# Performance work log

Measured on AMD Instinct MI355X. Metric: run time of the kernel, lower is better.

Reference implementation:

```python
import jax, jax.numpy as jnp
import numpy as np

MAX_HOPS = 2
N_NODES = 100000
N_EDGES = 1600000
D_FEAT = 64

def setup_inputs() -> dict:
    key = jax.random.key(0)
    k1, k2 = jax.random.split(key)
    x = jax.random.normal(k1, (N_NODES, D_FEAT), dtype=jnp.float32)
    edge_index = jax.random.randint(k2, (2, N_EDGES), 0, N_NODES, dtype=jnp.int64)
    hop_weights = jnp.ones((MAX_HOPS + 1,), dtype=jnp.float32)
    return {"x": x, "edge_index": edge_index, "hop_weights": hop_weights}

def reference(x, edge_index, hop_weights):
    num_nodes = x.shape[0]
    loops = jnp.arange(num_nodes, dtype=edge_index.dtype)
    row = jnp.concatenate([edge_index[0], loops])  # destination of scatter-add
    col = jnp.concatenate([edge_index[1], loops])  # gather source
    # symmetric GCN normalization D^{-1/2} A D^{-1/2} (degree computed over col, as in source)
    deg = jax.ops.segment_sum(jnp.ones_like(col, dtype=x.dtype), col, num_segments=num_nodes)
    deg_inv_sqrt = jnp.where(deg > 0, jax.lax.rsqrt(deg), 0.0)
    norm = deg_inv_sqrt[row] * deg_inv_sqrt[col]  # [E+N]
    w = jax.nn.softmax(hop_weights)
    result = w[0] * x
    current = x
    for hop in range(1, MAX_HOPS + 1):
        messages = current[col] * norm[:, None]  # irregular gather + scale
        current = jax.ops.segment_sum(messages, row, num_segments=num_nodes)  # scatter-add
        result = result + w[hop] * current
    return result
```

## Files before the change

### kernel.cpp

```cpp
#include <hip/hip_runtime.h>

#define NN 100000
#define NE 1600000
#define D 64

#define BKT 256
#define BROWS ((NN + BKT - 1) / BKT)
#define CAP 8192
#define PADCAP 12288
#define P1_NB 1024
#define P1_T 512
#define EPB ((NE + P1_NB - 1) / P1_NB)

typedef unsigned short u16;
typedef unsigned int u32;
typedef unsigned char u8;
typedef __attribute__((ext_vector_type(8))) unsigned short us8;


__device__ __forceinline__ float bf2f(u16 u) {
    union { u32 i; float f; } x; x.i = ((u32)u) << 16; return x.f;
}
__device__ __forceinline__ u16 f2bf(float f) {
    union { float f; u32 i; } x; x.f = f;
    u32 r = x.i + 0x7FFF + ((x.i >> 16) & 1);
    return (u16)(r >> 16);
}

__global__ void setup_kernel(const float* __restrict__ hw, float* __restrict__ wsm,
                             int* __restrict__ bcnt, int* __restrict__ bcnt2) {
    int t = threadIdx.x;
    if (t < BKT) bcnt[t] = 0;
    else if (t < 2 * BKT) bcnt2[t - BKT] = 0;
    else if (t == 2 * BKT) {
        float m = fmaxf(fmaxf(hw[0], hw[1]), hw[2]);
        float e0 = expf(hw[0] - m), e1 = expf(hw[1] - m), e2 = expf(hw[2] - m);
        float s = e0 + e1 + e2;
        wsm[0] = e0 / s; wsm[1] = e1 / s; wsm[2] = e2 / s;
    }
}

__global__ void __launch_bounds__(P1_T) fused_p1(const int* __restrict__ row,
                                                 const int* __restrict__ col,
                                                 int* __restrict__ bcnt,
                                                 int* __restrict__ bcnt2,
                                                 u32* __restrict__ buck,
                                                 u16* __restrict__ buck2) {
    __shared__ u32 st1[EPB];
    __shared__ u16 st2[EPB];
    __shared__ u8  sb1[EPB];
    __shared__ u8  sb2[EPB];
    __shared__ int h[BKT], h2[BKT];
    __shared__ int hoff[BKT], hoff2[BKT];
    __shared__ int resv[BKT], resv2[BKT];
    int t = threadIdx.x;
    int beg = blockIdx.x * EPB, end = min(NE, beg + EPB);
    int n = end - beg;
    for (int i = t; i < BKT; i += P1_T) { h[i] = 0; h2[i] = 0; }
    __syncthreads();
    for (int i = t; i < n; i += P1_T) {
        atomicAdd(&h[row[beg + i] / BROWS], 1);
        atomicAdd(&h2[col[beg + i] / BROWS], 1);
    }
    __syncthreads();
    int id = t & 255;
    int side = t >> 8;
    int* arr = (side == 0) ? h : h2;
    int myc = arr[id];
    for (int st = 1; st < BKT; st <<= 1) {
        int u = (id >= st) ? arr[id - st] : 0;
        __syncthreads();
        arr[id] += u;
        __syncthreads();
    }
    if (side == 0) {
        hoff[id] = h[id] - myc;
        resv[id] = atomicAdd(&bcnt[id], myc);
    } else {
        hoff2[id] = h2[id] - myc;
        resv2[id] = atomicAdd(&bcnt2[id], myc);
    }
    __syncthreads();
    if (t < BKT) h[t] = hoff[t];
    else h2[t - BKT] = hoff2[t - BKT];
    __syncthreads();
    for (int i = t; i < n; i += P1_T) {
        int r = row[beg + i], c = col[beg + i];
        int b1 = r / BROWS;
        int pos = atomicAdd(&h[b1], 1);
        st1[pos] = ((u32)(r - b1 * BROWS) << 17) | (u32)c;
        sb1[pos] = (u8)b1;
        int b2 = c / BROWS;
        int pos2 = atomicAdd(&h2[b2], 1);
        st2[pos2] = (u16)(c - b2 * BROWS);
        sb2[pos2] = (u8)b2;
    }
    __syncthreads();
    for (int i = t; i < n; i += P1_T) {
        int b1 = sb1[i];
        buck[(size_t)b1 * CAP + resv[b1] + (i - hoff[b1])] = st1[i];
        int b2 = sb2[i];
        buck2[(size_t)b2 * CAP + resv2[b2] + (i - hoff2[b2])] = st2[i];
    }
}

__global__ void __launch_bounds__(1024) build_both(const int* __restrict__ bcnt,
                                                   const u32* __restrict__ buck,
                                                   int* __restrict__ adjc,
                                                   int2* __restrict__ rowbe,
                                                   const int* __restrict__ bcnt2,
                                                   const u16* __restrict__ buck2,
                                                   float* __restrict__ dis,
                                                   float* __restrict__ dsi,
                                                   const float4* __restrict__ x,
                                                   ushort4* __restrict__ y1,
                                                   ushort4* __restrict__ y2) {
    __shared__ int ca[BROWS];
    __shared__ int wsum[16];
    int t = threadIdx.x;
    if (blockIdx.x < BKT) {
        int b = blockIdx.x;
        int row0 = b * BROWS;
        int nrows = min(BROWS, NN - row0);
        int cntb = bcnt2[b];
        const u16* eb = buck2 + (size_t)b * CAP;
        for (int i = t; i < nrows; i += 1024) ca[i] = 0;
        __syncthreads();
        for (int e = t; e < cntb; e += 1024)
            atomicAdd(&ca[eb[e]], 1);
        __syncthreads();
        if (t < nrows) {
            float dg = (float)(ca[t] + 1);
            dis[row0 + t] = rsqrtf(dg);
            dsi[row0 + t] = sqrtf(dg);
        }
        int items = nrows * 16;
        for (int i = t; i < items; i += 1024) {
            int r = i >> 4;
            float s = rsqrtf((float)(ca[r] + 1));
            int gidx = (row0 + r) * 16 + (i & 15);
            float4 v = x[gidx];
            ushort4 o;
            o.x = f2bf(s * v.x); o.y = f2bf(s * v.y); o.z = f2bf(s * v.z); o.w = f2bf(s * v.w);
            y1[gidx] = o;
        }
        if (b == BKT - 1 && t < 16) {
            ushort4 z = {0, 0, 0, 0};
            y1[NN * 16 + t] = z;
            y2[NN * 16 + t] = z;
        }
    } else {
        int b = blockIdx.x - BKT;
        int row0 = b * BROWS;
        int nrows = min(BROWS, NN - row0);
        int cntb = bcnt[b];
        const u32* eb = buck + (size_t)b * CAP;
        for (int i = t; i < nrows; i += 1024) ca[i] = 0;
        __syncthreads();
        for (int e = t; e < cntb; e += 1024)
            atomicAdd(&ca[eb[e] >> 17], 1);
        __syncthreads();
        int v = (t < nrows) ? ca[t] : 0;
        int vp = (v + 15) & ~15;
        int lane = t & 63, wv = t >> 6;
        int incl = vp;
        #pragma unroll
        for (int d = 1; d < 64; d <<= 1) {
            int u = __shfl_up(incl, d);
            if (lane >= d) incl += u;
        }
        if (lane == 63) wsum[wv] = incl;
        __syncthreads();
        if (t < 16) {
            int s = wsum[t];
            #pragma unroll
            for (int d = 1; d < 16; d <<= 1) {
                int u = __shfl_up(s, d, 16);
                if (t >= d) s += u;
            }
            wsum[t] = s;
        }
        __syncthreads();
        int excl = ((wv > 0) ? wsum[wv - 1] : 0) + incl - vp;
        if (t < nrows) {
            int base = b * PADCAP + excl;
            rowbe[row0 + t] = make_int2(base, base + vp);
            for (int p = base + v; p < base + vp; ++p) adjc[p] = NN;
            ca[t] = base;
        }
        __syncthreads();
        for (int e = t; e < cntb; e += 1024) {
            u32 p = eb[e];
            int pos = atomicAdd(&ca[p >> 17], 1);
            adjc[pos] = (int)(p & 0x1FFFFu);
        }
    }
}


__global__ void prop1_kernel(const int2* __restrict__ rowbe,
                             const int* __restrict__ adjc,
                             const float* __restrict__ dis,
                             const u16* __restrict__ y1,
                             u16* __restrict__ y2) {
    int tid = blockIdx.x * blockDim.x + threadIdx.x;
    int w = tid >> 6, l = tid & 63;
    int n = 2 * w + (l >> 5);
    int sg = (l >> 3) & 3;
    int ho = l & 7;
    int2 be = rowbe[n];
    float a[8] = {0.f, 0.f, 0.f, 0.f, 0.f, 0.f, 0.f, 0.f};
    #pragma unroll 2
    for (int j = be.x; j < be.y; j += 16) {
        int4 c = *(const int4*)&adjc[j + sg * 4];
        us8 v0 = *(const us8*)&y1[c.x * D + ho * 8];
        us8 v1 = *(const us8*)&y1[c.y * D + ho * 8];
        us8 v2 = *(const us8*)&y1[c.z * D + ho * 8];
        us8 v3 = *(const us8*)&y1[c.w * D + ho * 8];
        #pragma unroll
        for (int k = 0; k < 8; ++k)
            a[k] += (bf2f(v0[k]) + bf2f(v1[k])) + (bf2f(v2[k]) + bf2f(v3[k]));
    }
    #pragma unroll
    for (int k = 0; k < 8; ++k) {
        a[k] += __shfl_xor(a[k], 8);
        a[k] += __shfl_xor(a[k], 16);
    }
    if ((l & 31) < 8) {
        us8 s = *(const us8*)&y1[n * D + ho * 8];
        float di = dis[n], d2 = di * di;
        us8 o;
        #pragma unroll
        for (int k = 0; k < 8; ++k) o[k] = f2bf(d2 * (a[k] + bf2f(s[k])));
        *(us8*)&y2[n * D + ho * 8] = o;
    }
}

__global__ void prop2_kernel(const int2* __restrict__ rowbe,
                             const int* __restrict__ adjc,
                             const float* __restrict__ dis,
                             const float* __restrict__ dsi,
                             const u16* __restrict__ y1,
                             const u16* __restrict__ y2,
                             const float* __restrict__ wsm,
                             float* __restrict__ out) {
    int tid = blockIdx.x * blockDim.x + threadIdx.x;
    int w = tid >> 6, l = tid & 63;
    int n = 2 * w + (l >> 5);
    int sg = (l >> 3) & 3;
    int ho = l & 7;
    int2 be = rowbe[n];
    float a[8] = {0.f, 0.f, 0.f, 0.f, 0.f, 0.f, 0.f, 0.f};
    #pragma unroll 2
    for (int j = be.x; j < be.y; j += 16) {
        int4 c = *(const int4*)&adjc[j + sg * 4];
        us8 v0 = *(const us8*)&y2[c.x * D + ho * 8];
        us8 v1 = *(const us8*)&y2[c.y * D + ho * 8];
        us8 v2 = *(const us8*)&y2[c.z * D + ho * 8];
        us8 v3 = *(const us8*)&y2[c.w * D + ho * 8];
        #pragma unroll
        for (int k = 0; k < 8; ++k)
            a[k] += (bf2f(v0[k]) + bf2f(v1[k])) + (bf2f(v2[k]) + bf2f(v3[k]));
    }
    #pragma unroll
    for (int k = 0; k < 8; ++k) {
        a[k] += __shfl_xor(a[k], 8);
        a[k] += __shfl_xor(a[k], 16);
    }
    if ((l & 31) < 8) {
        us8 s1 = *(const us8*)&y1[n * D + ho * 8];
        us8 s2 = *(const us8*)&y2[n * D + ho * 8];
        float di = dis[n], ds = dsi[n];
        float w0 = wsm[0], w1 = wsm[1], w2 = wsm[2];
        float o[8];
        #pragma unroll
        for (int k = 0; k < 8; ++k) {
            float y2k = bf2f(s2[k]);
            o[k] = ds * (w0 * bf2f(s1[k]) + w1 * y2k) + w2 * (di * (a[k] + y2k));
        }
        float4 o0 = {o[0], o[1], o[2], o[3]};
        float4 o1 = {o[4], o[5], o[6], o[7]};
        *(float4*)&out[n * D + ho * 8] = o0;
        *(float4*)&out[n * D + ho * 8 + 4] = o1;
    }
}


extern "C" void kernel_launch(void* const* d_in, const int* in_sizes, int n_in,
                              void* d_out, int out_size, void* d_ws, size_t ws_size,
                              hipStream_t stream) {
    const float* x   = (const float*)d_in[0];
    const int*   ei  = (const int*)d_in[1];
    const float* hw  = (const float*)d_in[2];
    float*       out = (float*)d_out;

    const int* row = ei;
    const int* col = ei + NE;

    char* ws = (char*)d_ws;
    size_t off = 0;
    auto alloc = [&](size_t bytes) { size_t p = off; off += (bytes + 255) & ~(size_t)255; return p; };
    float* wsm    = (float*)(ws + alloc(16));
    int*   bcnt   = (int*)  (ws + alloc((size_t)BKT * 4));
    int*   bcnt2  = (int*)  (ws + alloc((size_t)BKT * 4));
    float* dis    = (float*)(ws + alloc((size_t)NN * 4));
    float* dsi    = (float*)(ws + alloc((size_t)NN * 4));
    u32*   buck   = (u32*)  (ws + alloc((size_t)BKT * CAP * 4));
    u16*   buck2  = (u16*)  (ws + alloc((size_t)BKT * CAP * 2));
    int*   adjc   = (int*)  (ws + alloc((size_t)BKT * PADCAP * 4));
    int2*  rowbe  = (int2*) (ws + alloc((size_t)NN * 8));
    u16*   y1     = (u16*)  (ws + alloc((size_t)(NN + 1) * D * 2));
    u16*   y2     = (u16*)  (ws + alloc((size_t)(NN + 1) * D * 2));

    setup_kernel<<<1, 1024, 0, stream>>>(hw, wsm, bcnt, bcnt2);
    fused_p1<<<P1_NB, P1_T, 0, stream>>>(row, col, bcnt, bcnt2, buck, buck2);
    build_both<<<2 * BKT, 1024, 0, stream>>>(bcnt, buck, adjc, rowbe,
                                             bcnt2, buck2, dis, dsi,
                                             (const float4*)x, (ushort4*)y1, (ushort4*)y2);

    const int prop_blocks = (NN / 2 + 3) / 4;
    prop1_kernel<<<prop_blocks, 256, 0, stream>>>(rowbe, adjc, dis, y1, y2);
    prop2_kernel<<<prop_blocks, 256, 0, stream>>>(rowbe, adjc, dis, dsi, y1, y2, wsm, out);
}
```

Before: 124.5 us.

## Use wavefront shuffle scan in edge bucketing and hoist self-loads in propagation

The bucketing kernel now runs 512 blocks of 1024 threads. Each thread keeps its up to four edges in registers, so row and col are no longer re-read from global memory. The block-wide prefix scan with repeated __syncthreads is replaced by a wavefront shuffle scan plus a small cross-wave combine. In both propagation kernels, the self-row feature and degree loads are hoisted before the neighbor loop so their latency overlaps the gathers, at the cost of extra registers and redundant loads in all lanes.

```diff
diff --git a/kernel.cpp b/kernel.cpp
--- a/kernel.cpp
+++ b/kernel.cpp
@@ -8,8 +8,8 @@
 #define BROWS ((NN + BKT - 1) / BKT)
 #define CAP 8192
 #define PADCAP 12288
-#define P1_NB 1024
-#define P1_T 512
+#define P1_NB 512
+#define P1_T 1024
 #define EPB ((NE + P1_NB - 1) / P1_NB)
 
 typedef unsigned short u16;
@@ -53,47 +53,70 @@
     __shared__ int h[BKT], h2[BKT];
     __shared__ int hoff[BKT], hoff2[BKT];
     __shared__ int resv[BKT], resv2[BKT];
+    __shared__ int wscan[8];
     int t = threadIdx.x;
     int beg = blockIdx.x * EPB, end = min(NE, beg + EPB);
     int n = end - beg;
-    for (int i = t; i < BKT; i += P1_T) { h[i] = 0; h2[i] = 0; }
-    __syncthreads();
-    for (int i = t; i < n; i += P1_T) {
-        atomicAdd(&h[row[beg + i] / BROWS], 1);
-        atomicAdd(&h2[col[beg + i] / BROWS], 1);
-    }
-    __syncthreads();
-    int id = t & 255;
-    int side = t >> 8;
-    int* arr = (side == 0) ? h : h2;
-    int myc = arr[id];
-    for (int st = 1; st < BKT; st <<= 1) {
-        int u = (id >= st) ? arr[id - st] : 0;
-        __syncthreads();
-        arr[id] += u;
-        __syncthreads();
-    }
-    if (side == 0) {
-        hoff[id] = h[id] - myc;
-        resv[id] = atomicAdd(&bcnt[id], myc);
-    } else {
-        hoff2[id] = h2[id] - myc;
-        resv2[id] = atomicAdd(&bcnt2[id], myc);
-    }
-    __syncthreads();
-    if (t < BKT) h[t] = hoff[t];
-    else h2[t - BKT] = hoff2[t - BKT];
-    __syncthreads();
-    for (int i = t; i < n; i += P1_T) {
-        int r = row[beg + i], c = col[beg + i];
-        int b1 = r / BROWS;
-        int pos = atomicAdd(&h[b1], 1);
-        st1[pos] = ((u32)(r - b1 * BROWS) << 17) | (u32)c;
-        sb1[pos] = (u8)b1;
-        int b2 = c / BROWS;
-        int pos2 = atomicAdd(&h2[b2], 1);
-        st2[pos2] = (u16)(c - b2 * BROWS);
-        sb2[pos2] = (u8)b2;
+    if (t < BKT) h[t] = 0;
+    else if (t < 2 * BKT) h2[t - BKT] = 0;
+    __syncthreads();
+    int rr[4], cc[4];
+    #pragma unroll
+    for (int k = 0; k < 4; ++k) {
+        int i = t + k * P1_T;
+        if (i < n) {
+            rr[k] = row[beg + i];
+            cc[k] = col[beg + i];
+            atomicAdd(&h[rr[k] / BROWS], 1);
+            atomicAdd(&h2[cc[k] / BROWS], 1);
+        } else {
+            rr[k] = -1; cc[k] = 0;
+        }
+    }
+    __syncthreads();
+    int id = t & 255, side = t >> 8, lane = t & 63, wv = (t >> 6) & 3;
+    int v = 0, incl = 0;
+    if (t < 2 * BKT) {
+        v = side ? h2[id] : h[id];
+        incl = v;
+        #pragma unroll
+        for (int d = 1; d < 64; d <<= 1) {
+            int u = __shfl_up(incl, d);
+            if (lane >= d) incl += u;
+        }
+        if (lane == 63) wscan[t >> 6] = incl;
+    }
+    __syncthreads();
+    if (t < 2 * BKT) {
+        int base = 0;
+        #pragma unroll
+        for (int k = 0; k < 3; ++k)
+            if (wv > k) base += wscan[(side << 2) | k];
+        int excl = base + incl - v;
+        if (side == 0) {
+            hoff[id] = excl;
+            resv[id] = atomicAdd(&bcnt[id], v);
+            h[id] = excl;
+        } else {
+            hoff2[id] = excl;
+            resv2[id] = atomicAdd(&bcnt2[id], v);
+            h2[id] = excl;
+        }
+    }
+    __syncthreads();
+    #pragma unroll
+    for (int k = 0; k < 4; ++k) {
+        if (rr[k] >= 0) {
+            int r = rr[k], c = cc[k];
+            int b1 = r / BROWS;
+            int pos = atomicAdd(&h[b1], 1);
+            st1[pos] = ((u32)(r - b1 * BROWS) << 17) | (u32)c;
+            sb1[pos] = (u8)b1;
+            int b2 = c / BROWS;
+            int pos2 = atomicAdd(&h2[b2], 1);
+            st2[pos2] = (u16)(c - b2 * BROWS);
+            sb2[pos2] = (u8)b2;
+        }
     }
     __syncthreads();
     for (int i = t; i < n; i += P1_T) {
@@ -139,9 +162,9 @@
             int r = i >> 4;
             float s = rsqrtf((float)(ca[r] + 1));
             int gidx = (row0 + r) * 16 + (i & 15);
-            float4 v = x[gidx];
+            float4 vv = x[gidx];
             ushort4 o;
-            o.x = f2bf(s * v.x); o.y = f2bf(s * v.y); o.z = f2bf(s * v.z); o.w = f2bf(s * v.w);
+            o.x = f2bf(s * vv.x); o.y = f2bf(s * vv.y); o.z = f2bf(s * vv.z); o.w = f2bf(s * vv.w);
             y1[gidx] = o;
         }
         if (b == BKT - 1 && t < 16) {
@@ -209,6 +232,8 @@
     int sg = (l >> 3) & 3;
     int ho = l & 7;
     int2 be = rowbe[n];
+    us8 s = *(const us8*)&y1[n * D + ho * 8];
+    float di = dis[n];
     float a[8] = {0.f, 0.f, 0.f, 0.f, 0.f, 0.f, 0.f, 0.f};
     #pragma unroll 2
     for (int j = be.x; j < be.y; j += 16) {
@@ -227,8 +252,7 @@
         a[k] += __shfl_xor(a[k], 16);
     }
     if ((l & 31) < 8) {
-        us8 s = *(const us8*)&y1[n * D + ho * 8];
-        float di = dis[n], d2 = di * di;
+        float d2 = di * di;
         us8 o;
         #pragma unroll
         for (int k = 0; k < 8; ++k) o[k] = f2bf(d2 * (a[k] + bf2f(s[k])));
@@ -250,6 +274,9 @@
     int sg = (l >> 3) & 3;
     int ho = l & 7;
     int2 be = rowbe[n];
+    us8 s1 = *(const us8*)&y1[n * D + ho * 8];
+    us8 s2 = *(const us8*)&y2[n * D + ho * 8];
+    float di = dis[n], ds = dsi[n];
     float a[8] = {0.f, 0.f, 0.f, 0.f, 0.f, 0.f, 0.f, 0.f};
     #pragma unroll 2
     for (int j = be.x; j < be.y; j += 16) {
@@ -268,9 +295,6 @@
         a[k] += __shfl_xor(a[k], 16);
     }
     if ((l & 31) < 8) {
-        us8 s1 = *(const us8*)&y1[n * D + ho * 8];
-        us8 s2 = *(const us8*)&y2[n * D + ho * 8];
-        float di = dis[n], ds = dsi[n];
         float w0 = wsm[0], w1 = wsm[1], w2 = wsm[2];
         float o[8];
         #pragma unroll
```

New measurement: 110.9 us. 1.12x faster.
